# Kernel optimization log

Measured on AMD Instinct MI355X. Metric: run time of the kernel, lower is better.

Reference implementation:

```python
import jax, jax.numpy as jnp
import numpy as np

V, D, NE, K, C = 500000, 128, 1000000, 8, 16
H1 = 8  # 2**l with l=3


def setup_inputs() -> dict:
    key = jax.random.key(0)
    ks = jax.random.split(key, 12)
    def w(k, shape, fan_in):
        return jax.random.normal(k, shape, jnp.float32) / np.sqrt(fan_in)
    return {
        "X": jax.random.normal(ks[0], (V, D), jnp.float32),
        "E": jax.random.randint(ks[1], (NE, K), 0, V, jnp.int64),
        "rv": jax.random.uniform(ks[2], (D,), jnp.float32),
        "W1": w(ks[3], (D, H1), D), "b1": jnp.zeros((H1,), jnp.float32),
        "W2": w(ks[4], (H1, H1), H1), "b2": jnp.zeros((H1,), jnp.float32),
        "W3": w(ks[5], (H1, C), H1), "b3": jnp.zeros((C,), jnp.float32),
        "fc_w": w(ks[6], (C, 1), C), "fc_b": jnp.zeros((1,), jnp.float32),
    }


def build_laplacian(X, E, rv):
    """HyperGCN fast Laplacian (no mediators): per hyperedge pick the
    argmax/argmin nodes of a random projection, connect them symmetrically
    with weight 1/|e|, add identity, symmetric D^-1/2 normalization.
    Returns (rows, cols, vals, diag_vals) of the sparse normalized adjacency."""
    n, k = X.shape[0], E.shape[1]
    proj = X @ rv                      # [V]
    p = proj[E]                        # [NE, K]
    ar = jnp.arange(E.shape[0])
    Se = E[ar, jnp.argmax(p, axis=1)]  # [NE]
    Ie = E[ar, jnp.argmin(p, axis=1)]  # [NE]
    rows = jnp.concatenate([Se, Ie])
    cols = jnp.concatenate([Ie, Se])
    vals = jnp.full(rows.shape, 1.0 / k, dtype=X.dtype)
    deg = jnp.ones((n,), X.dtype).at[rows].add(vals)  # +1 from identity
    dinv = jax.lax.rsqrt(deg)
    vals_n = vals * dinv[rows] * dinv[cols]
    diag_vals = dinv * dinv
    return rows, cols, vals_n, diag_vals


def spmm(rows, cols, vals, diag_vals, M):
    # (A_norm + normalized identity) @ M, M: [V, F]
    out = diag_vals[:, None] * M
    return out.at[rows].add(vals[:, None] * M[cols])


def reference(X, E, rv, W1, b1, W2, b2, W3, b3, fc_w, fc_b):
    rows, cols, vals, dvals = build_laplacian(X, E, rv)
    # dropout p=0.1 is a no-op in eval mode
    H = jax.nn.relu(spmm(rows, cols, vals, dvals, X @ W1) + b1)
    H = jax.nn.relu(spmm(rows, cols, vals, dvals, H @ W2) + b2)
    H = jax.nn.relu(spmm(rows, cols, vals, dvals, H @ W3) + b3)
    logits = (H @ fc_w + fc_b)[:, 0]   # [V]
    return jax.nn.sigmoid(logits)
```

## Files before the change

kernel.cpp:

```cpp
#include <hip/hip_runtime.h>
#include <hip/hip_bf16.h>

static constexpr int VN = 500000;
static constexpr int DD = 128;
static constexpr int NE = 1000000;
static constexpr int KE = 8;
static constexpr int CC = 16;
static constexpr int H1 = 8;
static constexpr int EW = 64;

typedef float fvec4 __attribute__((ext_vector_type(4)));

__global__ __launch_bounds__(256) void k_row(const float* __restrict__ X,
                                             const float* __restrict__ rv,
                                             const float* __restrict__ W1,
                                             float* __restrict__ proj,
                                             float* __restrict__ A,
                                             int* __restrict__ fill) {
    int v = blockIdx.x * 256 + threadIdx.x;
    if (v >= VN) return;
    fill[v] = 0;
    const fvec4* xr = reinterpret_cast<const fvec4*>(X + (size_t)v * DD);
    const float4* rr = reinterpret_cast<const float4*>(rv);
    float accP = 0.f;
    float accM[H1];
#pragma unroll
    for (int j = 0; j < H1; ++j) accM[j] = 0.f;
#pragma unroll 8
    for (int k = 0; k < DD / 4; ++k) {
        fvec4 x = __builtin_nontemporal_load(&xr[k]);
        float4 r = rr[k];
        accP += x.x * r.x + x.y * r.y + x.z * r.z + x.w * r.w;
#pragma unroll
        for (int q = 0; q < 4; ++q) {
            float xv = (q == 0) ? x.x : (q == 1) ? x.y : (q == 2) ? x.z : x.w;
            const float4 wa = *reinterpret_cast<const float4*>(W1 + (size_t)(k * 4 + q) * H1);
            const float4 wb = *reinterpret_cast<const float4*>(W1 + (size_t)(k * 4 + q) * H1 + 4);
            accM[0] += xv * wa.x; accM[1] += xv * wa.y;
            accM[2] += xv * wa.z; accM[3] += xv * wa.w;
            accM[4] += xv * wb.x; accM[5] += xv * wb.y;
            accM[6] += xv * wb.z; accM[7] += xv * wb.w;
        }
    }
    proj[v] = accP;
    float4* a4 = reinterpret_cast<float4*>(A + (size_t)v * H1);
    a4[0] = make_float4(accM[0], accM[1], accM[2], accM[3]);
    a4[1] = make_float4(accM[4], accM[5], accM[6], accM[7]);
}

__global__ __launch_bounds__(256) void k_place(const int* __restrict__ E,
                                               const float* __restrict__ proj,
                                               int* __restrict__ fill,
                                               int* __restrict__ ell) {
    int e = blockIdx.x * 256 + threadIdx.x;
    if (e >= NE) return;
    const int* er = E + (size_t)e * KE;
    int4 e0 = *reinterpret_cast<const int4*>(er);
    int4 e1 = *reinterpret_cast<const int4*>(er + 4);
    int ids[KE] = {e0.x, e0.y, e0.z, e0.w, e1.x, e1.y, e1.z, e1.w};
    float p[KE];
#pragma unroll
    for (int j = 0; j < KE; ++j) p[j] = proj[ids[j]];
    float bestMax = p[0], bestMin = p[0];
    int idMax = ids[0], idMin = ids[0];
#pragma unroll
    for (int j = 1; j < KE; ++j) {
        if (p[j] > bestMax) { bestMax = p[j]; idMax = ids[j]; }
        if (p[j] < bestMin) { bestMin = p[j]; idMin = ids[j]; }
    }
    int ps = atomicAdd(fill + idMax, 1);
    int pi = atomicAdd(fill + idMin, 1);
    ell[(size_t)idMax * EW + ps] = idMin;
    ell[(size_t)idMin * EW + pi] = idMax;
}

__global__ __launch_bounds__(256) void k_seed(const int* __restrict__ fill,
                                              float* __restrict__ dinv,
                                              float* __restrict__ A) {
    int v = blockIdx.x * 256 + threadIdx.x;
    if (v >= VN) return;
    float di = rsqrtf(1.0f + 0.125f * (float)fill[v]);
    dinv[v] = di;
    float4* ar = reinterpret_cast<float4*>(A + (size_t)v * H1);
    float4 a0 = ar[0], a1 = ar[1];
    ar[0] = make_float4(di * a0.x, di * a0.y, di * a0.z, di * a0.w);
    ar[1] = make_float4(di * a1.x, di * a1.y, di * a1.z, di * a1.w);
}

template <int FIN, int FOUT, int RSI, int RSO>
__global__ __launch_bounds__(256) void k_glayer(const int* __restrict__ ell,
                                                const int* __restrict__ fill,
                                                const float* __restrict__ dinv,
                                                const float* __restrict__ bias,
                                                const float* __restrict__ W,
                                                const float* __restrict__ Min,
                                                float* __restrict__ Mout) {
    int v = blockIdx.x * 256 + threadIdx.x;
    if (v >= VN) return;
    float own[FIN], s[FIN];
    const float4* mr = reinterpret_cast<const float4*>(Min + (size_t)v * RSI);
#pragma unroll
    for (int j = 0; j < FIN / 4; ++j) {
        float4 t = mr[j];
        own[4 * j] = t.x; own[4 * j + 1] = t.y;
        own[4 * j + 2] = t.z; own[4 * j + 3] = t.w;
    }
#pragma unroll
    for (int j = 0; j < FIN; ++j) s[j] = 0.f;
    int deg = fill[v];
    const int* row = ell + (size_t)v * EW;
    int base = 0;
    for (; base + 4 <= deg; base += 4) {
        int4 c4 = *reinterpret_cast<const int4*>(row + base);
        const float4* r0 = reinterpret_cast<const float4*>(Min + (size_t)c4.x * RSI);
        const float4* r1 = reinterpret_cast<const float4*>(Min + (size_t)c4.y * RSI);
        const float4* r2 = reinterpret_cast<const float4*>(Min + (size_t)c4.z * RSI);
        const float4* r3 = reinterpret_cast<const float4*>(Min + (size_t)c4.w * RSI);
        float4 t0[FIN / 4], t1[FIN / 4], t2[FIN / 4], t3[FIN / 4];
#pragma unroll
        for (int j = 0; j < FIN / 4; ++j) t0[j] = r0[j];
#pragma unroll
        for (int j = 0; j < FIN / 4; ++j) t1[j] = r1[j];
#pragma unroll
        for (int j = 0; j < FIN / 4; ++j) t2[j] = r2[j];
#pragma unroll
        for (int j = 0; j < FIN / 4; ++j) t3[j] = r3[j];
#pragma unroll
        for (int j = 0; j < FIN / 4; ++j) {
            s[4 * j]     += t0[j].x + t1[j].x + t2[j].x + t3[j].x;
            s[4 * j + 1] += t0[j].y + t1[j].y + t2[j].y + t3[j].y;
            s[4 * j + 2] += t0[j].z + t1[j].z + t2[j].z + t3[j].z;
            s[4 * j + 3] += t0[j].w + t1[j].w + t2[j].w + t3[j].w;
        }
    }
    for (; base < deg; ++base) {
        int c = row[base];
        const float4* cr = reinterpret_cast<const float4*>(Min + (size_t)c * RSI);
#pragma unroll
        for (int j = 0; j < FIN / 4; ++j) {
            float4 t = cr[j];
            s[4 * j] += t.x; s[4 * j + 1] += t.y;
            s[4 * j + 2] += t.z; s[4 * j + 3] += t.w;
        }
    }
    float di = dinv[v];
    float h[FIN];
#pragma unroll
    for (int j = 0; j < FIN; ++j) {
        float y = di * (own[j] + 0.125f * s[j]) + bias[j];
        h[j] = y > 0.f ? y : 0.f;
    }
#pragma unroll
    for (int c = 0; c < FOUT; ++c) {
        float m = 0.f;
#pragma unroll
        for (int j = 0; j < FIN; ++j) m += h[j] * W[j * FOUT + c];
        Mout[(size_t)v * RSO + c] = di * m;
    }
}

__global__ __launch_bounds__(256) void k_gfinal(const int* __restrict__ ell,
                                                const int* __restrict__ fill,
                                                const float* __restrict__ dinv,
                                                const float* __restrict__ b3,
                                                const float* __restrict__ fcw,
                                                const float* __restrict__ fcb,
                                                const float* __restrict__ Min,
                                                float* __restrict__ out) {
    int v = blockIdx.x * 256 + threadIdx.x;
    if (v >= VN) return;
    float own[CC], s[CC];
    const float4* mr = reinterpret_cast<const float4*>(Min + (size_t)v * CC);
#pragma unroll
    for (int j = 0; j < CC / 4; ++j) {
        float4 t = mr[j];
        own[4 * j] = t.x; own[4 * j + 1] = t.y;
        own[4 * j + 2] = t.z; own[4 * j + 3] = t.w;
    }
#pragma unroll
    for (int j = 0; j < CC; ++j) s[j] = 0.f;
    int deg = fill[v];
    const int* row = ell + (size_t)v * EW;
    int base = 0;
    for (; base + 2 <= deg; base += 2) {
        int c0 = row[base], c1 = row[base + 1];
        const float4* r0 = reinterpret_cast<const float4*>(Min + (size_t)c0 * CC);
        const float4* r1 = reinterpret_cast<const float4*>(Min + (size_t)c1 * CC);
        float4 t0[CC / 4], t1[CC / 4];
#pragma unroll
        for (int j = 0; j < CC / 4; ++j) t0[j] = r0[j];
#pragma unroll
        for (int j = 0; j < CC / 4; ++j) t1[j] = r1[j];
#pragma unroll
        for (int j = 0; j < CC / 4; ++j) {
            s[4 * j]     += t0[j].x + t1[j].x;
            s[4 * j + 1] += t0[j].y + t1[j].y;
            s[4 * j + 2] += t0[j].z + t1[j].z;
            s[4 * j + 3] += t0[j].w + t1[j].w;
        }
    }
    if (base < deg) {
        int c = row[base];
        const float4* cr = reinterpret_cast<const float4*>(Min + (size_t)c * CC);
#pragma unroll
        for (int j = 0; j < CC / 4; ++j) {
            float4 t = cr[j];
            s[4 * j] += t.x; s[4 * j + 1] += t.y;
            s[4 * j + 2] += t.z; s[4 * j + 3] += t.w;
        }
    }
    float di = dinv[v];
    float acc = fcb[0];
#pragma unroll
    for (int j = 0; j < CC; ++j) {
        float y = di * (own[j] + 0.125f * s[j]) + b3[j];
        float hh = y > 0.f ? y : 0.f;
        acc += hh * fcw[j];
    }
    out[v] = 1.f / (1.f + expf(-acc));
}

extern "C" void kernel_launch(void* const* d_in, const int* in_sizes, int n_in,
                              void* d_out, int out_size, void* d_ws, size_t ws_size,
                              hipStream_t stream) {
    const float* X   = (const float*)d_in[0];
    const int*   E   = (const int*)d_in[1];
    const float* rv  = (const float*)d_in[2];
    const float* W1  = (const float*)d_in[3];
    const float* b1  = (const float*)d_in[4];
    const float* W2  = (const float*)d_in[5];
    const float* b2  = (const float*)d_in[6];
    const float* W3  = (const float*)d_in[7];
    const float* b3  = (const float*)d_in[8];
    const float* fcw = (const float*)d_in[9];
    const float* fcb = (const float*)d_in[10];
    float* out = (float*)d_out;

    float* ws = (float*)d_ws;
    float* A    = ws;
    float* B    = ws + 4000000;
    float* C    = ws + 8000000;
    float* proj = ws + 16000000;
    float* dinv = ws + 16500000;
    int*   fill = (int*)(ws + 17000000);
    int*   ell  = (int*)(ws + 17500000);

    dim3 blk(256);
    int gV = (VN + 255) / 256;
    int gE = (NE + 255) / 256;

    k_row<<<gV, blk, 0, stream>>>(X, rv, W1, proj, A, fill);
    k_place<<<gE, blk, 0, stream>>>(E, proj, fill, ell);
    k_seed<<<gV, blk, 0, stream>>>(fill, dinv, A);

    k_glayer<8, 8, 8, 8><<<gV, blk, 0, stream>>>(ell, fill, dinv, b1, W2, A, B);
    k_glayer<8, 16, 8, 16><<<gV, blk, 0, stream>>>(ell, fill, dinv, b2, W3, B, C);
    k_gfinal<<<gV, blk, 0, stream>>>(ell, fill, dinv, b3, fcw, fcb, C, out);
}
```

Baseline: 374.9 us.

## Split each node's gather across four lanes and fold the seed pass into layer one

Each graph layer now assigns four threads per node. The threads split the neighbour list in a strided way and combine their partial sums with xor shuffles, which raises memory-level parallelism and evens out load imbalance across degrees. The separate seed kernel and dinv array are gone: degree normalisation is recomputed from fill with rsqrt, and in the first layer each neighbour is scaled on the fly. This adds an extra fill lookup per edge in that layer. Edge loads and ELL stores use nontemporal hints, and the stores are now bounded by the slot capacity.

```diff
diff --git a/kernel.cpp b/kernel.cpp
--- a/kernel.cpp
+++ b/kernel.cpp
@@ -10,6 +10,7 @@
 static constexpr int EW = 64;
 
 typedef float fvec4 __attribute__((ext_vector_type(4)));
+typedef int   ivec4 __attribute__((ext_vector_type(4)));
 
 __global__ __launch_bounds__(256) void k_row(const float* __restrict__ X,
                                              const float* __restrict__ rv,
@@ -54,9 +55,9 @@
                                                int* __restrict__ ell) {
     int e = blockIdx.x * 256 + threadIdx.x;
     if (e >= NE) return;
-    const int* er = E + (size_t)e * KE;
-    int4 e0 = *reinterpret_cast<const int4*>(er);
-    int4 e1 = *reinterpret_cast<const int4*>(er + 4);
+    const ivec4* er = reinterpret_cast<const ivec4*>(E + (size_t)e * KE);
+    ivec4 e0 = __builtin_nontemporal_load(&er[0]);
+    ivec4 e1 = __builtin_nontemporal_load(&er[1]);
     int ids[KE] = {e0.x, e0.y, e0.z, e0.w, e1.x, e1.y, e1.z, e1.w};
     float p[KE];
 #pragma unroll
@@ -70,120 +71,110 @@
     }
     int ps = atomicAdd(fill + idMax, 1);
     int pi = atomicAdd(fill + idMin, 1);
-    ell[(size_t)idMax * EW + ps] = idMin;
-    ell[(size_t)idMin * EW + pi] = idMax;
-}
-
-__global__ __launch_bounds__(256) void k_seed(const int* __restrict__ fill,
-                                              float* __restrict__ dinv,
-                                              float* __restrict__ A) {
-    int v = blockIdx.x * 256 + threadIdx.x;
+    if (ps < EW) __builtin_nontemporal_store(idMin, ell + (size_t)idMax * EW + ps);
+    if (pi < EW) __builtin_nontemporal_store(idMax, ell + (size_t)idMin * EW + pi);
+}
+
+template <int FIN, int FOUT, int RSI, int RSO, bool PRE>
+__global__ __launch_bounds__(256) void k_glayer4(const int* __restrict__ ell,
+                                                 const int* __restrict__ fill,
+                                                 const float* __restrict__ bias,
+                                                 const float* __restrict__ W,
+                                                 const float* __restrict__ Min,
+                                                 float* __restrict__ Mout) {
+    int t = blockIdx.x * 256 + threadIdx.x;
+    int v = t >> 2, g = t & 3;
     if (v >= VN) return;
-    float di = rsqrtf(1.0f + 0.125f * (float)fill[v]);
-    dinv[v] = di;
-    float4* ar = reinterpret_cast<float4*>(A + (size_t)v * H1);
-    float4 a0 = ar[0], a1 = ar[1];
-    ar[0] = make_float4(di * a0.x, di * a0.y, di * a0.z, di * a0.w);
-    ar[1] = make_float4(di * a1.x, di * a1.y, di * a1.z, di * a1.w);
-}
-
-template <int FIN, int FOUT, int RSI, int RSO>
-__global__ __launch_bounds__(256) void k_glayer(const int* __restrict__ ell,
-                                                const int* __restrict__ fill,
-                                                const float* __restrict__ dinv,
-                                                const float* __restrict__ bias,
-                                                const float* __restrict__ W,
-                                                const float* __restrict__ Min,
-                                                float* __restrict__ Mout) {
-    int v = blockIdx.x * 256 + threadIdx.x;
+    int deg = fill[v];
+    float di = rsqrtf(1.0f + 0.125f * (float)deg);
+    float s[FIN];
+#pragma unroll
+    for (int j = 0; j < FIN; ++j) s[j] = 0.f;
+    const int* row = ell + (size_t)v * EW;
+    int p = g;
+    for (; p + 4 < deg; p += 8) {
+        int c0 = row[p], c1 = row[p + 4];
+        float sc0 = 1.f, sc1 = 1.f;
+        if (!PRE) {
+            sc0 = rsqrtf(1.0f + 0.125f * (float)fill[c0]);
+            sc1 = rsqrtf(1.0f + 0.125f * (float)fill[c1]);
+        }
+        const float4* r0 = reinterpret_cast<const float4*>(Min + (size_t)c0 * RSI);
+        const float4* r1 = reinterpret_cast<const float4*>(Min + (size_t)c1 * RSI);
+        float4 t0[FIN / 4], t1[FIN / 4];
+#pragma unroll
+        for (int j = 0; j < FIN / 4; ++j) t0[j] = r0[j];
+#pragma unroll
+        for (int j = 0; j < FIN / 4; ++j) t1[j] = r1[j];
+#pragma unroll
+        for (int j = 0; j < FIN / 4; ++j) {
+            s[4 * j]     += sc0 * t0[j].x + sc1 * t1[j].x;
+            s[4 * j + 1] += sc0 * t0[j].y + sc1 * t1[j].y;
+            s[4 * j + 2] += sc0 * t0[j].z + sc1 * t1[j].z;
+            s[4 * j + 3] += sc0 * t0[j].w + sc1 * t1[j].w;
+        }
+    }
+    if (p < deg) {
+        int c = row[p];
+        float sc = 1.f;
+        if (!PRE) sc = rsqrtf(1.0f + 0.125f * (float)fill[c]);
+        const float4* cr = reinterpret_cast<const float4*>(Min + (size_t)c * RSI);
+#pragma unroll
+        for (int j = 0; j < FIN / 4; ++j) {
+            float4 tt = cr[j];
+            s[4 * j] += sc * tt.x; s[4 * j + 1] += sc * tt.y;
+            s[4 * j + 2] += sc * tt.z; s[4 * j + 3] += sc * tt.w;
+        }
+    }
+#pragma unroll
+    for (int j = 0; j < FIN; ++j) {
+        s[j] += __shfl_xor(s[j], 1);
+        s[j] += __shfl_xor(s[j], 2);
+    }
+    const float4* mr = reinterpret_cast<const float4*>(Min + (size_t)v * RSI);
+    float own[FIN];
+#pragma unroll
+    for (int j = 0; j < FIN / 4; ++j) {
+        float4 tt = mr[j];
+        own[4 * j] = tt.x; own[4 * j + 1] = tt.y;
+        own[4 * j + 2] = tt.z; own[4 * j + 3] = tt.w;
+    }
+    float osc = PRE ? 1.0f : di;
+    float h[FIN];
+#pragma unroll
+    for (int j = 0; j < FIN; ++j) {
+        float y = di * (osc * own[j] + 0.125f * s[j]) + bias[j];
+        h[j] = y > 0.f ? y : 0.f;
+    }
+#pragma unroll
+    for (int c = 0; c < FOUT / 4; ++c) {
+        int col = g + 4 * c;
+        float m = 0.f;
+#pragma unroll
+        for (int j = 0; j < FIN; ++j) m += h[j] * W[j * FOUT + col];
+        Mout[(size_t)v * RSO + col] = di * m;
+    }
+}
+
+__global__ __launch_bounds__(256) void k_gfinal4(const int* __restrict__ ell,
+                                                 const int* __restrict__ fill,
+                                                 const float* __restrict__ b3,
+                                                 const float* __restrict__ fcw,
+                                                 const float* __restrict__ fcb,
+                                                 const float* __restrict__ Min,
+                                                 float* __restrict__ out) {
+    int t = blockIdx.x * 256 + threadIdx.x;
+    int v = t >> 2, g = t & 3;
     if (v >= VN) return;
-    float own[FIN], s[FIN];
-    const float4* mr = reinterpret_cast<const float4*>(Min + (size_t)v * RSI);
-#pragma unroll
-    for (int j = 0; j < FIN / 4; ++j) {
-        float4 t = mr[j];
-        own[4 * j] = t.x; own[4 * j + 1] = t.y;
-        own[4 * j + 2] = t.z; own[4 * j + 3] = t.w;
-    }
-#pragma unroll
-    for (int j = 0; j < FIN; ++j) s[j] = 0.f;
     int deg = fill[v];
+    float di = rsqrtf(1.0f + 0.125f * (float)deg);
+    float s[CC];
+#pragma unroll
+    for (int j = 0; j < CC; ++j) s[j] = 0.f;
     const int* row = ell + (size_t)v * EW;
-    int base = 0;
-    for (; base + 4 <= deg; base += 4) {
-        int4 c4 = *reinterpret_cast<const int4*>(row + base);
-        const float4* r0 = reinterpret_cast<const float4*>(Min + (size_t)c4.x * RSI);
-        const float4* r1 = reinterpret_cast<const float4*>(Min + (size_t)c4.y * RSI);
-        const float4* r2 = reinterpret_cast<const float4*>(Min + (size_t)c4.z * RSI);
-        const float4* r3 = reinterpret_cast<const float4*>(Min + (size_t)c4.w * RSI);
-        float4 t0[FIN / 4], t1[FIN / 4], t2[FIN / 4], t3[FIN / 4];
-#pragma unroll
-        for (int j = 0; j < FIN / 4; ++j) t0[j] = r0[j];
-#pragma unroll
-        for (int j = 0; j < FIN / 4; ++j) t1[j] = r1[j];
-#pragma unroll
-        for (int j = 0; j < FIN / 4; ++j) t2[j] = r2[j];
-#pragma unroll
-        for (int j = 0; j < FIN / 4; ++j) t3[j] = r3[j];
-#pragma unroll
-        for (int j = 0; j < FIN / 4; ++j) {
-            s[4 * j]     += t0[j].x + t1[j].x + t2[j].x + t3[j].x;
-            s[4 * j + 1] += t0[j].y + t1[j].y + t2[j].y + t3[j].y;
-            s[4 * j + 2] += t0[j].z + t1[j].z + t2[j].z + t3[j].z;
-            s[4 * j + 3] += t0[j].w + t1[j].w + t2[j].w + t3[j].w;
-        }
-    }
-    for (; base < deg; ++base) {
-        int c = row[base];
-        const float4* cr = reinterpret_cast<const float4*>(Min + (size_t)c * RSI);
-#pragma unroll
-        for (int j = 0; j < FIN / 4; ++j) {
-            float4 t = cr[j];
-            s[4 * j] += t.x; s[4 * j + 1] += t.y;
-            s[4 * j + 2] += t.z; s[4 * j + 3] += t.w;
-        }
-    }
-    float di = dinv[v];
-    float h[FIN];
-#pragma unroll
-    for (int j = 0; j < FIN; ++j) {
-        float y = di * (own[j] + 0.125f * s[j]) + bias[j];
-        h[j] = y > 0.f ? y : 0.f;
-    }
-#pragma unroll
-    for (int c = 0; c < FOUT; ++c) {
-        float m = 0.f;
-#pragma unroll
-        for (int j = 0; j < FIN; ++j) m += h[j] * W[j * FOUT + c];
-        Mout[(size_t)v * RSO + c] = di * m;
-    }
-}
-
-__global__ __launch_bounds__(256) void k_gfinal(const int* __restrict__ ell,
-                                                const int* __restrict__ fill,
-                                                const float* __restrict__ dinv,
-                                                const float* __restrict__ b3,
-                                                const float* __restrict__ fcw,
-                                                const float* __restrict__ fcb,
-                                                const float* __restrict__ Min,
-                                                float* __restrict__ out) {
-    int v = blockIdx.x * 256 + threadIdx.x;
-    if (v >= VN) return;
-    float own[CC], s[CC];
-    const float4* mr = reinterpret_cast<const float4*>(Min + (size_t)v * CC);
-#pragma unroll
-    for (int j = 0; j < CC / 4; ++j) {
-        float4 t = mr[j];
-        own[4 * j] = t.x; own[4 * j + 1] = t.y;
-        own[4 * j + 2] = t.z; own[4 * j + 3] = t.w;
-    }
-#pragma unroll
-    for (int j = 0; j < CC; ++j) s[j] = 0.f;
-    int deg = fill[v];
-    const int* row = ell + (size_t)v * EW;
-    int base = 0;
-    for (; base + 2 <= deg; base += 2) {
-        int c0 = row[base], c1 = row[base + 1];
+    int p = g;
+    for (; p + 4 < deg; p += 8) {
+        int c0 = row[p], c1 = row[p + 4];
         const float4* r0 = reinterpret_cast<const float4*>(Min + (size_t)c0 * CC);
         const float4* r1 = reinterpret_cast<const float4*>(Min + (size_t)c1 * CC);
         float4 t0[CC / 4], t1[CC / 4];
@@ -199,25 +190,40 @@
             s[4 * j + 3] += t0[j].w + t1[j].w;
         }
     }
-    if (base < deg) {
-        int c = row[base];
+    if (p < deg) {
+        int c = row[p];
         const float4* cr = reinterpret_cast<const float4*>(Min + (size_t)c * CC);
 #pragma unroll
         for (int j = 0; j < CC / 4; ++j) {
-            float4 t = cr[j];
-            s[4 * j] += t.x; s[4 * j + 1] += t.y;
-            s[4 * j + 2] += t.z; s[4 * j + 3] += t.w;
-        }
-    }
-    float di = dinv[v];
-    float acc = fcb[0];
+            float4 tt = cr[j];
+            s[4 * j] += tt.x; s[4 * j + 1] += tt.y;
+            s[4 * j + 2] += tt.z; s[4 * j + 3] += tt.w;
+        }
+    }
 #pragma unroll
     for (int j = 0; j < CC; ++j) {
-        float y = di * (own[j] + 0.125f * s[j]) + b3[j];
+        s[j] += __shfl_xor(s[j], 1);
+        s[j] += __shfl_xor(s[j], 2);
+    }
+    const float4* mr = reinterpret_cast<const float4*>(Min + (size_t)v * CC);
+    float own[CC];
+#pragma unroll
+    for (int j = 0; j < CC / 4; ++j) {
+        float4 tt = mr[j];
+        own[4 * j] = tt.x; own[4 * j + 1] = tt.y;
+        own[4 * j + 2] = tt.z; own[4 * j + 3] = tt.w;
+    }
+    float acc = 0.f;
+#pragma unroll
+    for (int c = 0; c < CC / 4; ++c) {
+        int col = g + 4 * c;
+        float y = di * (own[col] + 0.125f * s[col]) + b3[col];
         float hh = y > 0.f ? y : 0.f;
-        acc += hh * fcw[j];
-    }
-    out[v] = 1.f / (1.f + expf(-acc));
+        acc += hh * fcw[col];
+    }
+    acc += __shfl_xor(acc, 1);
+    acc += __shfl_xor(acc, 2);
+    if (g == 0) out[v] = 1.f / (1.f + expf(-(acc + fcb[0])));
 }
 
 extern "C" void kernel_launch(void* const* d_in, const int* in_sizes, int n_in,
@@ -241,19 +247,18 @@
     float* B    = ws + 4000000;
     float* C    = ws + 8000000;
     float* proj = ws + 16000000;
-    float* dinv = ws + 16500000;
-    int*   fill = (int*)(ws + 17000000);
-    int*   ell  = (int*)(ws + 17500000);
+    int*   fill = (int*)(ws + 16500000);
+    int*   ell  = (int*)(ws + 17000000);
 
     dim3 blk(256);
-    int gV = (VN + 255) / 256;
-    int gE = (NE + 255) / 256;
+    int gV  = (VN + 255) / 256;
+    int gE  = (NE + 255) / 256;
+    int gV4 = (VN * 4 + 255) / 256;
 
     k_row<<<gV, blk, 0, stream>>>(X, rv, W1, proj, A, fill);
     k_place<<<gE, blk, 0, stream>>>(E, proj, fill, ell);
-    k_seed<<<gV, blk, 0, stream>>>(fill, dinv, A);
-
-    k_glayer<8, 8, 8, 8><<<gV, blk, 0, stream>>>(ell, fill, dinv, b1, W2, A, B);
-    k_glayer<8, 16, 8, 16><<<gV, blk, 0, stream>>>(ell, fill, dinv, b2, W3, B, C);
-    k_gfinal<<<gV, blk, 0, stream>>>(ell, fill, dinv, b3, fcw, fcb, C, out);
-}
+
+    k_glayer4<8, 8, 8, 8, false><<<gV4, blk, 0, stream>>>(ell, fill, b1, W2, A, B);
+    k_glayer4<8, 16, 8, 16, true><<<gV4, blk, 0, stream>>>(ell, fill, b2, W3, B, C);
+    k_gfinal4<<<gV4, blk, 0, stream>>>(ell, fill, b3, fcw, fcb, C, out);
+}
```

Result: slower. 385.9 us (+2.9%).
